# Performance work log

Measured on AMD Instinct MI355X. Metric: run time of the kernel, lower is better.

Reference implementation:

```python
import jax, jax.numpy as jnp
import numpy as np

HEADS = 4
HID = 128            # hidden_channels
D = HID // HEADS     # per-head dim = 32
IN = 128
OUT = 64
NEG = 0.2            # PyG HANConv default negative_slope
N_AUTHOR = 100000
N_PAPER = 200000
E = 1000000


def setup_inputs() -> dict:
    key = jax.random.key(0)
    ks = jax.random.split(key, 24)
    g = lambda i, shape, s=1.0: jax.random.normal(ks[i], shape, jnp.float32) * s
    ri = lambda i, hi: jax.random.randint(ks[i], (E,), 0, hi, dtype=jnp.int64)
    sp = float(1.0 / np.sqrt(IN))
    sh = float(1.0 / np.sqrt(HID))
    return dict(
        x_author=g(0, (N_AUTHOR, IN)),
        x_paper=g(1, (N_PAPER, IN)),
        writes_src=ri(13, N_AUTHOR), writes_dst=ri(14, N_PAPER),
        writtenby_src=ri(15, N_PAPER), writtenby_dst=ri(16, N_AUTHOR),
        cites_src=ri(17, N_PAPER), cites_dst=ri(18, N_PAPER),
        W_proj_author=g(2, (IN, HID), sp), b_proj_author=jnp.zeros((HID,), jnp.float32),
        W_proj_paper=g(3, (IN, HID), sp), b_proj_paper=jnp.zeros((HID,), jnp.float32),
        att_src_writes=g(4, (HEADS, D), sh), att_dst_writes=g(5, (HEADS, D), sh),
        att_src_writtenby=g(6, (HEADS, D), sh), att_dst_writtenby=g(7, (HEADS, D), sh),
        att_src_cites=g(8, (HEADS, D), sh), att_dst_cites=g(9, (HEADS, D), sh),
        W_k=g(10, (HID, HID), sh), b_k=jnp.zeros((HID,), jnp.float32),
        q=g(11, (HID,), sh),
        W_lin=g(12, (HID, OUT), sh), b_lin=jnp.zeros((OUT,), jnp.float32),
    )


def _edge_conv(x_src, x_dst, att_s, att_d, src, dst, n_dst):
    # x_src: [Ns,H,D], x_dst: [Nd,H,D]; gather-attend-(segment softmax)-scatter
    a_s = jnp.einsum('nhd,hd->nh', x_src, att_s)[src]   # [E,H]
    a_d = jnp.einsum('nhd,hd->nh', x_dst, att_d)[dst]   # [E,H]
    alpha = jax.nn.leaky_relu(a_s + a_d, NEG)
    m = jax.ops.segment_max(alpha, dst, num_segments=n_dst)      # [Nd,H]
    ex = jnp.exp(alpha - m[dst])
    den = jax.ops.segment_sum(ex, dst, num_segments=n_dst)
    alpha = ex / (den[dst] + 1e-16)
    msg = (x_src[src] * alpha[:, :, None]).reshape(-1, HID)      # [E,HID]
    out = jax.ops.segment_sum(msg, dst, num_segments=n_dst)      # [Nd,HID]
    return jax.nn.relu(out)


def _group(outs, q, W_k, b_k):
    # semantic-level attention over edge types (PyG HANConv `group`)
    out = jnp.stack(outs)                                         # [T,N,HID]
    score = (q * jnp.tanh(out @ W_k + b_k).mean(axis=1)).sum(-1)  # [T]
    attn = jax.nn.softmax(score)
    return jnp.einsum('t,tnc->nc', attn, out)


def reference(x_author, x_paper, writes_src, writes_dst, writtenby_src,
              writtenby_dst, cites_src, cites_dst, W_proj_author,
              b_proj_author, W_proj_paper, b_proj_paper, att_src_writes,
              att_dst_writes, att_src_writtenby, att_dst_writtenby,
              att_src_cites, att_dst_cites, W_k, b_k, q, W_lin, b_lin):
    h_a = (x_author @ W_proj_author + b_proj_author).reshape(-1, HEADS, D)
    h_p = (x_paper @ W_proj_paper + b_proj_paper).reshape(-1, HEADS, D)
    o_writes = _edge_conv(h_a, h_p, att_src_writes, att_dst_writes,
                          writes_src, writes_dst, N_PAPER)
    o_wb = _edge_conv(h_p, h_a, att_src_writtenby, att_dst_writtenby,
                      writtenby_src, writtenby_dst, N_AUTHOR)
    o_cites = _edge_conv(h_p, h_p, att_src_cites, att_dst_cites,
                         cites_src, cites_dst, N_PAPER)
    out_author = _group([o_wb], q, W_k, b_k)
    out_paper = _group([o_writes, o_cites], q, W_k, b_k)
    # final per-node-type shared Linear (HANModel.lin)
    return (out_author @ W_lin + b_lin, out_paper @ W_lin + b_lin)
```

## Files before the change

### kernel.cpp

```cpp
#include <hip/hip_runtime.h>
#include <hip/hip_bf16.h>


#define HEADS 4
#define DH 32
#define HID 128
#define IN_F 128
#define OUT_F 64
#define NEG 0.2f

typedef unsigned short u16;
typedef unsigned int u32;
typedef __attribute__((ext_vector_type(8))) short short8;
typedef __attribute__((ext_vector_type(4))) float f32x4;

__device__ __forceinline__ float us2f(u16 u){ return __uint_as_float(((u32)u) << 16); }
__device__ __forceinline__ u16 f2us(float f){
  u32 u = __float_as_uint(f);
  u += 0x7fffu + ((u >> 16) & 1u);
  return (u16)(u >> 16);
}
__device__ __forceinline__ float fin(float v){ return (fabsf(v) < 1e30f) ? v : 0.f; }
__device__ __forceinline__ u16 san16(u16 r){ return (((r >> 7) & 0xff) == 0xff) ? (u16)0 : r; }
__device__ __forceinline__ float ldf(const void* p, size_t i, int wide){
  float v = wide ? ((const float*)p)[i] : us2f(((const u16*)p)[i]);
  return fin(v);
}
__device__ __forceinline__ u16 ld16(const void* p, size_t i, int wide){
  if (wide) return f2us(fin(((const float*)p)[i]));
  return san16(((const u16*)p)[i]);
}
__device__ __forceinline__ int ld_idx(const int* __restrict__ p, int e, int sh, int n){
  int v = p[(size_t)e << sh];
  return v < 0 ? 0 : (v >= n ? n - 1 : v);
}

__global__ void detect_float_width(const u16* __restrict__ x, int n, int* __restrict__ flag)
{
  __shared__ int cnt;
  if (threadIdx.x == 0) cnt = 0;
  __syncthreads();
  int local = 0;
  for (int i = threadIdx.x; i < n; i += blockDim.x) {
    int e = (x[i] >> 7) & 0xff;
    if (e == 0 || (e >= 100 && e <= 150)) local++;
  }
  atomicAdd(&cnt, local);
  __syncthreads();
  if (threadIdx.x == 0) *flag = (cnt < (n * 9) / 10) ? 1 : 0;
}
__global__ void detect_idx_width(const int* __restrict__ s, int n, int* __restrict__ flag)
{
  __shared__ int any;
  if (threadIdx.x == 0) any = 0;
  __syncthreads();
  for (int i = threadIdx.x; i < n; i += blockDim.x)
    if (s[2 * i + 1] != 0) atomicOr(&any, 1);
  __syncthreads();
  if (threadIdx.x == 0) *flag = any ? 0 : 1;
}

template<int N1, int N2>
__device__ __forceinline__ void stage_B(const void* W1, const void* W2, int wide, u16* Bt)
{
  constexpr int NC = N1 + N2;
  for (int i = threadIdx.x; i < 128 * NC; i += 256) {
    int k = i / NC, c = i - k * NC;
    u16 v;
    if constexpr (N2 == 0) {
      v = ld16(W1, (size_t)k * N1 + c, wide);
    } else {
      v = (c < N1) ? ld16(W1, (size_t)k * N1 + c, wide)
                   : ld16(W2, (size_t)k * N2 + (c - N1), wide);
    }
    u32 boff = ((u32)c << 8) + (((u32)(k << 1)) ^ (((u32)(c & 7)) << 4));
    *(u16*)((char*)Bt + boff) = v;
  }
}

__device__ __forceinline__ short8 ldsB(const u16* Bt, int t, int lane, int kk)
{
  const int c = (t << 4) + (lane & 15);
  const u32 boff = ((u32)c << 8) +
      (((u32)(((lane >> 4) << 4) + (kk << 6))) ^ (((u32)(c & 7)) << 4));
  return *(const short8*)((const char*)Bt + boff);
}

__device__ __forceinline__ short8 ldA_x(const void* x, size_t rb, int kg, int kk, int wide)
{
  short8 v;
  const size_t base = rb + (size_t)(kg * 8 + kk * 32);
  if (wide) {
    const float* p = (const float*)x + base;
    const float4 f0 = *(const float4*)p;
    const float4 f1 = *(const float4*)(p + 4);
    v[0] = (short)f2us(fin(f0.x)); v[1] = (short)f2us(fin(f0.y));
    v[2] = (short)f2us(fin(f0.z)); v[3] = (short)f2us(fin(f0.w));
    v[4] = (short)f2us(fin(f1.x)); v[5] = (short)f2us(fin(f1.y));
    v[6] = (short)f2us(fin(f1.z)); v[7] = (short)f2us(fin(f1.w));
  } else {
    const short8 raw = *(const short8*)((const u16*)x + base);
#pragma unroll
    for (int j = 0; j < 8; ++j) v[j] = (short)san16((u16)raw[j]);
  }
  return v;
}

__device__ __forceinline__ short8 ldA_o(const u16* o, size_t rb, int kg, int kk)
{
  return *(const short8*)(o + rb + (size_t)(kg * 8 + kk * 32));
}

__global__ __launch_bounds__(256) void proj_mfma(
    const void* __restrict__ x, const void* __restrict__ W,
    const void* __restrict__ b, u16* __restrict__ h, int N,
    const int* __restrict__ flag_f)
{
  const int wide = *flag_f;
  __shared__ u16 Bt[128 * 128];
  stage_B<HID, 0>(W, nullptr, wide, Bt);
  __syncthreads();
  const int w = threadIdx.x >> 6, lane = threadIdx.x & 63;
  const int r16 = lane & 15, kg = lane >> 4;
  float bv[8];
#pragma unroll
  for (int t = 0; t < 8; ++t) bv[t] = ldf(b, (t << 4) + r16, wide);
  const int nstrips = (N + 63) >> 6;
  for (int sidx = blockIdx.x; sidx < nstrips; sidx += gridDim.x) {
    const int rowbase = (sidx << 6) + (w << 4);
    int arow = rowbase + r16;
    if (arow >= N) arow = N - 1;
    const size_t rb = (size_t)arow * IN_F;
    f32x4 acc[8];
#pragma unroll
    for (int t = 0; t < 8; ++t) acc[t] = (f32x4){0.f, 0.f, 0.f, 0.f};
#pragma unroll
    for (int kk = 0; kk < 4; ++kk) {
      const short8 a = ldA_x(x, rb, kg, kk, wide);
#pragma unroll
      for (int t = 0; t < 8; ++t)
        acc[t] = __builtin_amdgcn_mfma_f32_16x16x32_bf16(a, ldsB(Bt, t, lane, kk), acc[t], 0, 0, 0);
    }
#pragma unroll
    for (int t = 0; t < 8; ++t) {
      const int col = (t << 4) + r16;
#pragma unroll
      for (int j = 0; j < 4; ++j) {
        const int row = rowbase + (kg << 2) + j;
        if (row < N) h[(size_t)row * HID + col] = f2us(acc[t][j] + bv[t]);
      }
    }
  }
}

__global__ __launch_bounds__(256) void fused_post(
    const u16* __restrict__ o, int rows, const void* __restrict__ Wk,
    const void* __restrict__ bk, const void* __restrict__ Wlin,
    float* __restrict__ S, u16* __restrict__ P,
    const int* __restrict__ flag_f)
{
  const int wide = *flag_f;
  __shared__ u16 Bt[192 * 128];
  __shared__ float sred[4][HID];
  stage_B<HID, OUT_F>(Wk, Wlin, wide, Bt);
  __syncthreads();
  const int w = threadIdx.x >> 6, lane = threadIdx.x & 63;
  const int r16 = lane & 15, kg = lane >> 4;
  float bkv[8];
#pragma unroll
  for (int t = 0; t < 8; ++t) bkv[t] = ldf(bk, (t << 4) + r16, wide);
  float scs[8] = {0.f, 0.f, 0.f, 0.f, 0.f, 0.f, 0.f, 0.f};
  const int nstrips = (rows + 63) >> 6;
  for (int sidx = blockIdx.x; sidx < nstrips; sidx += gridDim.x) {
    const int rowbase = (sidx << 6) + (w << 4);
    int arow = rowbase + r16;
    if (arow >= rows) arow = rows - 1;
    const size_t rb = (size_t)arow * HID;
    f32x4 acc[12];
#pragma unroll
    for (int t = 0; t < 12; ++t) acc[t] = (f32x4){0.f, 0.f, 0.f, 0.f};
#pragma unroll
    for (int kk = 0; kk < 4; ++kk) {
      const short8 a = ldA_o(o, rb, kg, kk);
#pragma unroll
      for (int t = 0; t < 12; ++t)
        acc[t] = __builtin_amdgcn_mfma_f32_16x16x32_bf16(a, ldsB(Bt, t, lane, kk), acc[t], 0, 0, 0);
    }
#pragma unroll
    for (int t = 0; t < 8; ++t) {
#pragma unroll
      for (int j = 0; j < 4; ++j) {
        const int row = rowbase + (kg << 2) + j;
        if (row < rows) scs[t] += tanhf(acc[t][j] + bkv[t]);
      }
    }
#pragma unroll
    for (int t = 8; t < 12; ++t) {
      const int col = ((t - 8) << 4) + r16;
#pragma unroll
      for (int j = 0; j < 4; ++j) {
        const int row = rowbase + (kg << 2) + j;
        if (row < rows) P[(size_t)row * OUT_F + col] = f2us(acc[t][j]);
      }
    }
  }
#pragma unroll
  for (int t = 0; t < 8; ++t) {
    float v = scs[t];
    v += __shfl_xor(v, 16);
    v += __shfl_xor(v, 32);
    if (kg == 0) sred[w][(t << 4) + r16] = v;
  }
  __syncthreads();
  if (threadIdx.x < HID) {
    float v = sred[0][threadIdx.x] + sred[1][threadIdx.x] +
              sred[2][threadIdx.x] + sred[3][threadIdx.x];
    atomicAdd(&S[threadIdx.x], v);
  }
}

__global__ __launch_bounds__(256) void author_mfma(
    const u16* __restrict__ o, int rows, int node0,
    const void* __restrict__ Wlin, const void* __restrict__ blin,
    void* __restrict__ out, const int* __restrict__ flag_f)
{
  const int wide = *flag_f;
  __shared__ u16 Bt[64 * 128];
  stage_B<OUT_F, 0>(Wlin, nullptr, wide, Bt);
  __syncthreads();
  const int w = threadIdx.x >> 6, lane = threadIdx.x & 63;
  const int r16 = lane & 15, kg = lane >> 4;
  float bv[4];
#pragma unroll
  for (int t = 0; t < 4; ++t) bv[t] = ldf(blin, (t << 4) + r16, wide);
  const int nstrips = (rows + 63) >> 6;
  for (int sidx = blockIdx.x; sidx < nstrips; sidx += gridDim.x) {
    const int rowbase = (sidx << 6) + (w << 4);
    int arow = rowbase + r16;
    if (arow >= rows) arow = rows - 1;
    const size_t rb = (size_t)arow * HID;
    f32x4 acc[4];
#pragma unroll
    for (int t = 0; t < 4; ++t) acc[t] = (f32x4){0.f, 0.f, 0.f, 0.f};
#pragma unroll
    for (int kk = 0; kk < 4; ++kk) {
      const short8 a = ldA_o(o, rb, kg, kk);
#pragma unroll
      for (int t = 0; t < 4; ++t)
        acc[t] = __builtin_amdgcn_mfma_f32_16x16x32_bf16(a, ldsB(Bt, t, lane, kk), acc[t], 0, 0, 0);
    }
#pragma unroll
    for (int t = 0; t < 4; ++t) {
      const int col = (t << 4) + r16;
#pragma unroll
      for (int j = 0; j < 4; ++j) {
        const int row = rowbase + (kg << 2) + j;
        if (row < rows) {
          const float val = acc[t][j] + bv[t];
          const size_t oi = (size_t)(node0 + row) * OUT_F + col;
          if (wide) ((float*)out)[oi] = val;
          else      ((u16*)out)[oi] = f2us(val);
        }
      }
    }
  }
}

__global__ __launch_bounds__(256) void compute_a2(
    const u16* __restrict__ h, const void* __restrict__ att1,
    const void* __restrict__ att2, float* __restrict__ a1,
    float* __restrict__ a2, int N, const int* __restrict__ flag_f)
{
  const int wide = *flag_f;
  __shared__ float s1[HID], s2[HID];
  if (threadIdx.x < HID) {
    s1[threadIdx.x] = ldf(att1, threadIdx.x, wide);
    s2[threadIdx.x] = ldf(att2, threadIdx.x, wide);
  }
  __syncthreads();
  int t = blockIdx.x * 256 + threadIdx.x;
  if (t >= N * HEADS) return;
  int n = t >> 2, hh = t & 3;
  const u16* p = h + (size_t)n * HID + hh * DH;
  float acc1 = 0.f, acc2 = 0.f;
#pragma unroll
  for (int d = 0; d < DH; ++d) {
    float f = us2f(p[d]);
    acc1 += f * s1[hh * DH + d];
    acc2 += f * s2[hh * DH + d];
  }
  a1[t] = fin(acc1);
  a2[t] = fin(acc2);
}

__global__ __launch_bounds__(256) void hist_kernel(
    const int* __restrict__ dst, int E, const int* __restrict__ flag_i,
    int Nd, int* __restrict__ deg)
{
  int e = blockIdx.x * 256 + threadIdx.x;
  if (e >= E) return;
  int sh = *flag_i;
  int d = ld_idx(dst, e, sh, Nd);
  atomicAdd(&deg[d], 1);
}

__global__ __launch_bounds__(256) void scan1_kernel(
    const int* __restrict__ deg, int Nd, int* __restrict__ rowptr,
    int* __restrict__ blksum)
{
  __shared__ int ssum[256];
  int base = blockIdx.x * 1024;
  int t = threadIdx.x;
  int idx0 = base + t * 4;
  int v[4];
#pragma unroll
  for (int j = 0; j < 4; ++j) v[j] = (idx0 + j < Nd) ? deg[idx0 + j] : 0;
  int tsum = v[0] + v[1] + v[2] + v[3];
  ssum[t] = tsum;
  __syncthreads();
  for (int ofs = 1; ofs < 256; ofs <<= 1) {
    int x = (t >= ofs) ? ssum[t - ofs] : 0;
    __syncthreads();
    ssum[t] += x;
    __syncthreads();
  }
  if (t == 255) blksum[blockIdx.x] = ssum[255];
  int run = ssum[t] - tsum;
#pragma unroll
  for (int j = 0; j < 4; ++j) {
    if (idx0 + j < Nd) rowptr[idx0 + j] = run;
    run += v[j];
  }
}

__global__ void scan2_kernel(int* __restrict__ blksum, int nb)
{
  if (threadIdx.x == 0 && blockIdx.x == 0) {
    int run = 0;
    for (int b = 0; b < nb; ++b) { int t = blksum[b]; blksum[b] = run; run += t; }
  }
}

__global__ __launch_bounds__(256) void scan3_kernel(
    int* __restrict__ rowptr, int* __restrict__ cursor,
    const int* __restrict__ blksum, int Nd, int E)
{
  int i = blockIdx.x * 256 + threadIdx.x;
  if (i < Nd) {
    int v = rowptr[i] + blksum[i >> 10];
    rowptr[i] = v;
    cursor[i] = v;
  }
  if (i == 0) rowptr[Nd] = E;
}

__global__ __launch_bounds__(256) void reorder_kernel(
    const int* __restrict__ src, const int* __restrict__ dst, int E,
    const int* __restrict__ flag_i, int Ns, int Nd,
    int* __restrict__ cursor, int* __restrict__ csr_src)
{
  int e = blockIdx.x * 256 + threadIdx.x;
  if (e >= E) return;
  int sh = *flag_i;
  int d = ld_idx(dst, e, sh, Nd);
  int s = ld_idx(src, e, sh, Ns);
  int pos = atomicAdd(&cursor[d], 1);
  csr_src[pos] = s;
}

__global__ __launch_bounds__(256) void gather_conv(
    const int* __restrict__ rowptr, const int* __restrict__ csr_src,
    const float* __restrict__ a_s, const float* __restrict__ a_d,
    const u16* __restrict__ h_src, u16* __restrict__ o,
    int lo, int rows)
{
  int wid = (blockIdx.x * 256 + threadIdx.x) >> 6;
  if (wid >= rows) return;
  int n = lo + wid;
  int lane = threadIdx.x & 63;
  int hh = lane >> 4;
  int start = rowptr[n], end = rowptr[n + 1];
  float ad = a_d[(size_t)n * HEADS + hh];
  float m = -1e30f, den = 0.f, n0 = 0.f, n1 = 0.f;
  int e = start;
  for (; e + 4 <= end; e += 4) {
    int s0 = csr_src[e],     s1 = csr_src[e + 1];
    int s2 = csr_src[e + 2], s3 = csr_src[e + 3];
    float x0 = a_s[(size_t)s0 * HEADS + hh] + ad;
    float x1 = a_s[(size_t)s1 * HEADS + hh] + ad;
    float x2 = a_s[(size_t)s2 * HEADS + hh] + ad;
    float x3 = a_s[(size_t)s3 * HEADS + hh] + ad;
    ushort2 h0 = *(const ushort2*)(h_src + (size_t)s0 * HID + 2 * lane);
    ushort2 h1 = *(const ushort2*)(h_src + (size_t)s1 * HID + 2 * lane);
    ushort2 h2 = *(const ushort2*)(h_src + (size_t)s2 * HID + 2 * lane);
    ushort2 h3 = *(const ushort2*)(h_src + (size_t)s3 * HID + 2 * lane);
    x0 = (x0 > 0.f) ? x0 : NEG * x0;
    x1 = (x1 > 0.f) ? x1 : NEG * x1;
    x2 = (x2 > 0.f) ? x2 : NEG * x2;
    x3 = (x3 > 0.f) ? x3 : NEG * x3;
    float mloc = fmaxf(fmaxf(x0, x1), fmaxf(x2, x3));
    float mn = fmaxf(m, mloc);
    float sc = __expf(m - mn);
    float e0 = __expf(x0 - mn), e1 = __expf(x1 - mn);
    float e2 = __expf(x2 - mn), e3 = __expf(x3 - mn);
    den = den * sc + ((e0 + e1) + (e2 + e3));
    n0  = n0 * sc + (e0 * us2f(h0.x) + e1 * us2f(h1.x))
                  + (e2 * us2f(h2.x) + e3 * us2f(h3.x));
    n1  = n1 * sc + (e0 * us2f(h0.y) + e1 * us2f(h1.y))
                  + (e2 * us2f(h2.y) + e3 * us2f(h3.y));
    m = mn;
  }
  for (; e < end; ++e) {
    int s = csr_src[e];
    float x = a_s[(size_t)s * HEADS + hh] + ad;
    ushort2 hv = *(const ushort2*)(h_src + (size_t)s * HID + 2 * lane);
    x = (x > 0.f) ? x : NEG * x;
    float mn = fmaxf(m, x);
    float sc = __expf(m - mn);
    float ex = __expf(x - mn);
    den = den * sc + ex;
    n0  = n0 * sc + ex * us2f(hv.x);
    n1  = n1 * sc + ex * us2f(hv.y);
    m = mn;
  }
  float inv = 1.f / (den + 1e-16f);
  ushort2 st;
  st.x = f2us(fmaxf(n0 * inv, 0.f));
  st.y = f2us(fmaxf(n1 * inv, 0.f));
  *(ushort2*)(o + (size_t)wid * HID + 2 * lane) = st;
}

__global__ void score_softmax(const float* __restrict__ S, const void* __restrict__ q,
                              float* __restrict__ attn, float invN,
                              const int* __restrict__ flag_f)
{
  if (threadIdx.x == 0 && blockIdx.x == 0) {
    const int wide = *flag_f;
    float s0 = 0.f, s1 = 0.f;
    for (int c = 0; c < HID; ++c) {
      float qc = ldf(q, c, wide);
      s0 += qc * S[c] * invN;
      s1 += qc * S[HID + c] * invN;
    }
    float m = fmaxf(s0, s1);
    float e0 = __expf(s0 - m), e1 = __expf(s1 - m);
    attn[0] = e0 / (e0 + e1);
    attn[1] = e1 / (e0 + e1);
  }
}

__global__ __launch_bounds__(256) void combine_paper(
    const u16* __restrict__ Pw, const u16* __restrict__ Pc,
    const float* __restrict__ attn, const void* __restrict__ blin,
    void* __restrict__ out, size_t elem_off, int N,
    const int* __restrict__ flag_f)
{
  int t = blockIdx.x * 256 + threadIdx.x;
  if (t >= N * 16) return;
  const int wide = *flag_f;
  int n = t >> 4, cq = t & 15;
  const float a0 = attn[0], a1 = attn[1];
  size_t i = (size_t)n * OUT_F + cq * 4;
  ushort4 w4 = *(const ushort4*)&Pw[i];
  ushort4 c4 = *(const ushort4*)&Pc[i];
  float v[4];
  v[0] = a0 * us2f(w4.x) + a1 * us2f(c4.x) + ldf(blin, cq * 4 + 0, wide);
  v[1] = a0 * us2f(w4.y) + a1 * us2f(c4.y) + ldf(blin, cq * 4 + 1, wide);
  v[2] = a0 * us2f(w4.z) + a1 * us2f(c4.z) + ldf(blin, cq * 4 + 2, wide);
  v[3] = a0 * us2f(w4.w) + a1 * us2f(c4.w) + ldf(blin, cq * 4 + 3, wide);
  size_t oi = elem_off + i;
  if (wide) {
    float4 ov = {v[0], v[1], v[2], v[3]};
    *(float4*)&((float*)out)[oi] = ov;
  } else {
    ushort4 ov;
    ov.x = f2us(v[0]); ov.y = f2us(v[1]); ov.z = f2us(v[2]); ov.w = f2us(v[3]);
    *(ushort4*)&((u16*)out)[oi] = ov;
  }
}

extern "C" void kernel_launch(void* const* d_in, const int* in_sizes, int n_in,
                              void* d_out, int out_size, void* d_ws, size_t ws_size,
                              hipStream_t stream)
{
  const int NA = in_sizes[0] / IN_F;
  const int NP = in_sizes[1] / IN_F;
  const int E_w = in_sizes[2], E_wb = in_sizes[4], E_c = in_sizes[6];
  int Emax = E_w > E_wb ? E_w : E_wb;
  if (E_c > Emax) Emax = E_c;

  const void* x_a   = d_in[0];
  const void* x_p   = d_in[1];
  const int* w_src  = (const int*)d_in[2];
  const int* w_dst  = (const int*)d_in[3];
  const int* wb_src = (const int*)d_in[4];
  const int* wb_dst = (const int*)d_in[5];
  const int* c_src  = (const int*)d_in[6];
  const int* c_dst  = (const int*)d_in[7];
  const void* W_pa  = d_in[8];
  const void* b_pa  = d_in[9];
  const void* W_pp  = d_in[10];
  const void* b_pp  = d_in[11];
  const void* at_s_w  = d_in[12];
  const void* at_d_w  = d_in[13];
  const void* at_s_wb = d_in[14];
  const void* at_d_wb = d_in[15];
  const void* at_s_c  = d_in[16];
  const void* at_d_c  = d_in[17];
  const void* W_k   = d_in[18];
  const void* b_k   = d_in[19];
  const void* q     = d_in[20];
  const void* W_lin = d_in[21];
  const void* b_lin = d_in[22];

  char* ws = (char*)d_ws;
  size_t off = 0;
  auto alloc = [&](size_t bytes) -> void* {
    void* p = ws + off;
    off += (bytes + 255) & ~(size_t)255;
    return p;
  };
  int*   flag_f = (int*)alloc(4);
  int*   flag_i = (int*)alloc(4);
  float* attn   = (float*)alloc(8 * 4);
  float* S      = (float*)alloc(2 * HID * 4);
  u16*   h_a    = (u16*)alloc((size_t)NA * HID * 2);
  u16*   h_p    = (u16*)alloc((size_t)NP * HID * 2);
  float* aA_ws  = (float*)alloc((size_t)NA * HEADS * 4);
  float* aA_wbd = (float*)alloc((size_t)NA * HEADS * 4);
  float* aP_wd  = (float*)alloc((size_t)NP * HEADS * 4);
  float* aP_wbs = (float*)alloc((size_t)NP * HEADS * 4);
  float* aP_cs  = (float*)alloc((size_t)NP * HEADS * 4);
  float* aP_cd  = (float*)alloc((size_t)NP * HEADS * 4);
  u16*   Pw16   = (u16*)alloc((size_t)NP * OUT_F * 2);
  u16*   Pc16   = (u16*)alloc((size_t)NP * OUT_F * 2);
  int*   deg    = (int*)alloc((size_t)NP * 4);
  int*   rowptr = (int*)alloc(((size_t)NP + 1) * 4);
  int*   cursor = (int*)alloc((size_t)NP * 4);
  int*   blksum = (int*)alloc(1024);
  int*   csrsrc = (int*)alloc((size_t)Emax * 4);
  u16*   o16    = (u16*)(ws + off);
  size_t o_bytes = (ws_size > off) ? (ws_size - off) : 0;
  long long cap = (long long)(o_bytes / ((size_t)HID * 2));
  int rc = (int)(cap > NP ? NP : cap);
  rc &= ~63;
  if (rc < 64) rc = 64;

  detect_float_width<<<1, 256, 0, stream>>>((const u16*)x_a, 4096, flag_f);
  detect_idx_width<<<1, 256, 0, stream>>>(w_src, 512, flag_i);

  {
    int gA = (NA + 63) / 64; if (gA > 1024) gA = 1024;
    int gP = (NP + 63) / 64; if (gP > 1024) gP = 1024;
    proj_mfma<<<gA, 256, 0, stream>>>(x_a, W_pa, b_pa, h_a, NA, flag_f);
    proj_mfma<<<gP, 256, 0, stream>>>(x_p, W_pp, b_pp, h_p, NP, flag_f);
  }
  compute_a2<<<(NA * HEADS + 255) / 256, 256, 0, stream>>>(h_a, at_s_w, at_d_wb, aA_ws, aA_wbd, NA, flag_f);
  compute_a2<<<(NP * HEADS + 255) / 256, 256, 0, stream>>>(h_p, at_d_w, at_s_wb, aP_wd, aP_wbs, NP, flag_f);
  compute_a2<<<(NP * HEADS + 255) / 256, 256, 0, stream>>>(h_p, at_s_c, at_d_c, aP_cs, aP_cd, NP, flag_f);

  hipMemsetAsync(S, 0, 2 * HID * 4, stream);

  auto build_csr = [&](const int* srcp, const int* dstp, int Ecnt, int Ns, int Nd) {
    hipMemsetAsync(deg, 0, (size_t)Nd * 4, stream);
    hist_kernel<<<(Ecnt + 255) / 256, 256, 0, stream>>>(dstp, Ecnt, flag_i, Nd, deg);
    int nb = (Nd + 1023) / 1024;
    scan1_kernel<<<nb, 256, 0, stream>>>(deg, Nd, rowptr, blksum);
    scan2_kernel<<<1, 64, 0, stream>>>(blksum, nb);
    scan3_kernel<<<(Nd + 255) / 256, 256, 0, stream>>>(rowptr, cursor, blksum, Nd, Ecnt);
    reorder_kernel<<<(Ecnt + 255) / 256, 256, 0, stream>>>(srcp, dstp, Ecnt, flag_i, Ns, Nd, cursor, csrsrc);
  };

  build_csr(wb_src, wb_dst, E_wb, NP, NA);
  for (int lo = 0; lo < NA; lo += rc) {
    int rows = (NA - lo < rc) ? (NA - lo) : rc;
    gather_conv<<<(rows + 3) / 4, 256, 0, stream>>>(rowptr, csrsrc, aP_wbs, aA_wbd, h_p, o16, lo, rows);
    int g = (rows + 63) / 64; if (g > 1024) g = 1024;
    author_mfma<<<g, 256, 0, stream>>>(o16, rows, lo, W_lin, b_lin, d_out, flag_f);
  }

  build_csr(w_src, w_dst, E_w, NA, NP);
  for (int lo = 0; lo < NP; lo += rc) {
    int rows = (NP - lo < rc) ? (NP - lo) : rc;
    gather_conv<<<(rows + 3) / 4, 256, 0, stream>>>(rowptr, csrsrc, aA_ws, aP_wd, h_a, o16, lo, rows);
    int g = (rows + 63) / 64; if (g > 768) g = 768;
    fused_post<<<g, 256, 0, stream>>>(o16, rows, W_k, b_k, W_lin, S, Pw16 + (size_t)lo * OUT_F, flag_f);
  }

  build_csr(c_src, c_dst, E_c, NP, NP);
  for (int lo = 0; lo < NP; lo += rc) {
    int rows = (NP - lo < rc) ? (NP - lo) : rc;
    gather_conv<<<(rows + 3) / 4, 256, 0, stream>>>(rowptr, csrsrc, aP_cs, aP_cd, h_p, o16, lo, rows);
    int g = (rows + 63) / 64; if (g > 768) g = 768;
    fused_post<<<g, 256, 0, stream>>>(o16, rows, W_k, b_k, W_lin, S + HID, Pc16 + (size_t)lo * OUT_F, flag_f);
  }

  score_softmax<<<1, 64, 0, stream>>>(S, q, attn, 1.0f / (float)NP, flag_f);
  combine_paper<<<((size_t)NP * 16 + 255) / 256, 256, 0, stream>>>(Pw16, Pc16, attn, b_lin, d_out, (size_t)NA * OUT_F, NP, flag_f);
}
```

Baseline: 1.360 ms.

## Split fused post-projection into colsum and linear kernels with fast tanh

Splits the fused Wk+Wlin kernel into two kernels, one computing the tanh column sums and one computing the Wlin projection. This shrinks the shared memory per block and the accumulator registers, and adds launch-bounds hints for two blocks per CU. tanhf is replaced by an exp-based fast approximation, and the grid cap rises to 1024. In exchange the o16 buffer is read twice and one extra launch is added per chunk.

```diff
diff --git a/kernel.cpp b/kernel.cpp
--- a/kernel.cpp
+++ b/kernel.cpp
@@ -22,6 +22,10 @@
 }
 __device__ __forceinline__ float fin(float v){ return (fabsf(v) < 1e30f) ? v : 0.f; }
 __device__ __forceinline__ u16 san16(u16 r){ return (((r >> 7) & 0xff) == 0xff) ? (u16)0 : r; }
+__device__ __forceinline__ float ftanh(float x){
+  float t = __expf(fminf(fmaxf(2.f * x, -30.f), 30.f));
+  return __fdividef(t - 1.f, t + 1.f);
+}
 __device__ __forceinline__ float ldf(const void* p, size_t i, int wide){
   float v = wide ? ((const float*)p)[i] : us2f(((const u16*)p)[i]);
   return fin(v);
@@ -111,7 +115,7 @@
   return *(const short8*)(o + rb + (size_t)(kg * 8 + kk * 32));
 }
 
-__global__ __launch_bounds__(256) void proj_mfma(
+__global__ __launch_bounds__(256, 2) void proj_mfma(
     const void* __restrict__ x, const void* __restrict__ W,
     const void* __restrict__ b, u16* __restrict__ h, int N,
     const int* __restrict__ flag_f)
@@ -153,16 +157,15 @@
   }
 }
 
-__global__ __launch_bounds__(256) void fused_post(
+__global__ __launch_bounds__(256, 2) void colsum_mfma(
     const u16* __restrict__ o, int rows, const void* __restrict__ Wk,
-    const void* __restrict__ bk, const void* __restrict__ Wlin,
-    float* __restrict__ S, u16* __restrict__ P,
+    const void* __restrict__ bk, float* __restrict__ S,
     const int* __restrict__ flag_f)
 {
   const int wide = *flag_f;
-  __shared__ u16 Bt[192 * 128];
+  __shared__ u16 Bt[128 * 128];
   __shared__ float sred[4][HID];
-  stage_B<HID, OUT_F>(Wk, Wlin, wide, Bt);
+  stage_B<HID, 0>(Wk, nullptr, wide, Bt);
   __syncthreads();
   const int w = threadIdx.x >> 6, lane = threadIdx.x & 63;
   const int r16 = lane & 15, kg = lane >> 4;
@@ -176,14 +179,14 @@
     int arow = rowbase + r16;
     if (arow >= rows) arow = rows - 1;
     const size_t rb = (size_t)arow * HID;
-    f32x4 acc[12];
-#pragma unroll
-    for (int t = 0; t < 12; ++t) acc[t] = (f32x4){0.f, 0.f, 0.f, 0.f};
+    f32x4 acc[8];
+#pragma unroll
+    for (int t = 0; t < 8; ++t) acc[t] = (f32x4){0.f, 0.f, 0.f, 0.f};
 #pragma unroll
     for (int kk = 0; kk < 4; ++kk) {
       const short8 a = ldA_o(o, rb, kg, kk);
 #pragma unroll
-      for (int t = 0; t < 12; ++t)
+      for (int t = 0; t < 8; ++t)
         acc[t] = __builtin_amdgcn_mfma_f32_16x16x32_bf16(a, ldsB(Bt, t, lane, kk), acc[t], 0, 0, 0);
     }
 #pragma unroll
@@ -191,16 +194,7 @@
 #pragma unroll
       for (int j = 0; j < 4; ++j) {
         const int row = rowbase + (kg << 2) + j;
-        if (row < rows) scs[t] += tanhf(acc[t][j] + bkv[t]);
-      }
-    }
-#pragma unroll
-    for (int t = 8; t < 12; ++t) {
-      const int col = ((t - 8) << 4) + r16;
-#pragma unroll
-      for (int j = 0; j < 4; ++j) {
-        const int row = rowbase + (kg << 2) + j;
-        if (row < rows) P[(size_t)row * OUT_F + col] = f2us(acc[t][j]);
+        if (row < rows) scs[t] += ftanh(acc[t][j] + bkv[t]);
       }
     }
   }
@@ -219,7 +213,45 @@
   }
 }
 
-__global__ __launch_bounds__(256) void author_mfma(
+__global__ __launch_bounds__(256, 2) void linW_mfma(
+    const u16* __restrict__ o, int rows, const void* __restrict__ Wlin,
+    u16* __restrict__ P, const int* __restrict__ flag_f)
+{
+  const int wide = *flag_f;
+  __shared__ u16 Bt[64 * 128];
+  stage_B<OUT_F, 0>(Wlin, nullptr, wide, Bt);
+  __syncthreads();
+  const int w = threadIdx.x >> 6, lane = threadIdx.x & 63;
+  const int r16 = lane & 15, kg = lane >> 4;
+  const int nstrips = (rows + 63) >> 6;
+  for (int sidx = blockIdx.x; sidx < nstrips; sidx += gridDim.x) {
+    const int rowbase = (sidx << 6) + (w << 4);
+    int arow = rowbase + r16;
+    if (arow >= rows) arow = rows - 1;
+    const size_t rb = (size_t)arow * HID;
+    f32x4 acc[4];
+#pragma unroll
+    for (int t = 0; t < 4; ++t) acc[t] = (f32x4){0.f, 0.f, 0.f, 0.f};
+#pragma unroll
+    for (int kk = 0; kk < 4; ++kk) {
+      const short8 a = ldA_o(o, rb, kg, kk);
+#pragma unroll
+      for (int t = 0; t < 4; ++t)
+        acc[t] = __builtin_amdgcn_mfma_f32_16x16x32_bf16(a, ldsB(Bt, t, lane, kk), acc[t], 0, 0, 0);
+    }
+#pragma unroll
+    for (int t = 0; t < 4; ++t) {
+      const int col = (t << 4) + r16;
+#pragma unroll
+      for (int j = 0; j < 4; ++j) {
+        const int row = rowbase + (kg << 2) + j;
+        if (row < rows) P[(size_t)row * OUT_F + col] = f2us(acc[t][j]);
+      }
+    }
+  }
+}
+
+__global__ __launch_bounds__(256, 2) void author_mfma(
     const u16* __restrict__ o, int rows, int node0,
     const void* __restrict__ Wlin, const void* __restrict__ blin,
     void* __restrict__ out, const int* __restrict__ flag_f)
@@ -583,16 +615,18 @@
   for (int lo = 0; lo < NP; lo += rc) {
     int rows = (NP - lo < rc) ? (NP - lo) : rc;
     gather_conv<<<(rows + 3) / 4, 256, 0, stream>>>(rowptr, csrsrc, aA_ws, aP_wd, h_a, o16, lo, rows);
-    int g = (rows + 63) / 64; if (g > 768) g = 768;
-    fused_post<<<g, 256, 0, stream>>>(o16, rows, W_k, b_k, W_lin, S, Pw16 + (size_t)lo * OUT_F, flag_f);
+    int g = (rows + 63) / 64; if (g > 1024) g = 1024;
+    colsum_mfma<<<g, 256, 0, stream>>>(o16, rows, W_k, b_k, S, flag_f);
+    linW_mfma<<<g, 256, 0, stream>>>(o16, rows, W_lin, Pw16 + (size_t)lo * OUT_F, flag_f);
   }
 
   build_csr(c_src, c_dst, E_c, NP, NP);
   for (int lo = 0; lo < NP; lo += rc) {
     int rows = (NP - lo < rc) ? (NP - lo) : rc;
     gather_conv<<<(rows + 3) / 4, 256, 0, stream>>>(rowptr, csrsrc, aP_cs, aP_cd, h_p, o16, lo, rows);
-    int g = (rows + 63) / 64; if (g > 768) g = 768;
-    fused_post<<<g, 256, 0, stream>>>(o16, rows, W_k, b_k, W_lin, S + HID, Pc16 + (size_t)lo * OUT_F, flag_f);
+    int g = (rows + 63) / 64; if (g > 1024) g = 1024;
+    colsum_mfma<<<g, 256, 0, stream>>>(o16, rows, W_k, b_k, S + HID, flag_f);
+    linW_mfma<<<g, 256, 0, stream>>>(o16, rows, W_lin, Pc16 + (size_t)lo * OUT_F, flag_f);
   }
 
   score_softmax<<<1, 64, 0, stream>>>(S, q, attn, 1.0f / (float)NP, flag_f);
```

After: 1.287 ms. 1.06x faster.
